# Optimization experiments

Hardware: AMD Instinct MI355X
Metric: run time of the kernel (lower is better)

## Reference

```python
import jax, jax.numpy as jnp
import numpy as np

N = 50000      # num atoms
E = 800000     # num edges
F = 64         # atom_fea_len
NBR = 64       # nbr_fea_len
NCONV = 3
T = 4096       # pooled target atoms
STATE = 2
VOCAB = 100
EPS = 1e-5


def setup_inputs() -> dict:
    key = jax.random.key(0)
    ks = jax.random.split(key, 20)
    Z = 2 * F + NBR  # concat message width
    inp = {
        "x_types": jax.random.randint(ks[0], (N,), 0, VOCAB),
        "edge_index": jax.random.randint(ks[1], (2, E), 0, N),
        "edge_attr": jax.random.normal(ks[2], (E, NBR), dtype=jnp.float32),
        "target": jax.random.randint(ks[3], (T,), 0, N),
        "emb": jax.random.normal(ks[4], (VOCAB, F), dtype=jnp.float32),
        "Wc": jax.random.normal(ks[5], (NCONV, F, Z), dtype=jnp.float32) * 0.05,
        "bc": jnp.zeros((NCONV, F), jnp.float32),
        "Wf": jax.random.normal(ks[6], (NCONV, 1, Z), dtype=jnp.float32) * 0.05,
        "bf": jnp.zeros((NCONV, 1), jnp.float32),
        "g1": jnp.ones((NCONV, F), jnp.float32),
        "b1": jnp.zeros((NCONV, F), jnp.float32),
        "g2": jnp.ones((NCONV, F), jnp.float32),
        "b2": jnp.zeros((NCONV, F), jnp.float32),
        "Wfc": jax.random.normal(ks[7], (F, F), dtype=jnp.float32) * 0.05,
        "bfc": jnp.zeros((F,), jnp.float32),
        "Ws": jax.random.normal(ks[8], (STATE, F), dtype=jnp.float32) * 0.05,
        "bs": jnp.zeros((STATE,), jnp.float32),
    }
    return inp


def _segment_softmax(logits, idx, n):
    # per-target-node softmax over variable-size edge neighborhoods
    m = jax.ops.segment_max(logits, idx, num_segments=n)
    m = jnp.where(jnp.isfinite(m), m, 0.0)
    e = jnp.exp(logits - m[idx])
    s = jax.ops.segment_sum(e, idx, num_segments=n)
    return e / (s[idx] + 1e-16)


def _batchnorm(x, gamma, beta):
    # training-mode BatchNorm1d: biased batch stats over dim 0
    mu = x.mean(0)
    var = x.var(0)
    return (x - mu) * jax.lax.rsqrt(var + EPS) * gamma + beta


def reference(x_types, edge_index, edge_attr, target, emb, Wc, bc, Wf, bf,
              g1, b1, g2, b2, Wfc, bfc, Ws, bs):
    x = emb[x_types]                      # [N, F]
    # flow='target_to_source': i = edge_index[0] (aggregate here), j = edge_index[1]
    idx_i = edge_index[0]
    idx_j = edge_index[1]
    ones = jnp.ones((edge_index.shape[1],), x.dtype)
    cnt = jax.ops.segment_sum(ones, idx_i, num_segments=x.shape[0])
    denom = jnp.maximum(cnt, 1.0)[:, None]
    for l in range(NCONV):
        z = jnp.concatenate([x[idx_i], x[idx_j], edge_attr], axis=1)  # [E, 2F+NBR]
        core = jax.nn.relu(_batchnorm(z @ Wc[l].T + bc[l], g1[l], b1[l]))  # [E, F]
        filt = (z @ Wf[l].T + bf[l])[:, 0]                                  # [E]
        alpha = _segment_softmax(filt, idx_i, x.shape[0])[:, None]          # [E, 1]
        agg = jax.ops.segment_sum(alpha * core, idx_i, num_segments=x.shape[0]) / denom
        x = jax.nn.relu(_batchnorm(agg, g2[l], b2[l]) + x)
    h = jax.nn.relu(x[target])            # [T, F]
    h = jax.nn.relu(h @ Wfc.T + bfc)
    logits = h @ Ws.T + bs                # [T, STATE]
    return jax.nn.softmax(logits, axis=-1)
```

## Files before the change

kernel.cpp:

```cpp
#include <hip/hip_runtime.h>
#include <math.h>

#define N_ATOMS 50000
#define N_EDGES 800000
#define F 64
#define Z 192
#define NCONV 3
#define T_TGT 4096
#define EPS 1e-5f
#define SLOTS 64
#define NB_SCAN 196
#define TILE_E 128
#define TPB_TILES 5
#define NBLK_MM 1250

typedef __attribute__((ext_vector_type(4))) float f32x4;
typedef __attribute__((ext_vector_type(8))) short s16x8;
typedef __attribute__((ext_vector_type(8))) __bf16 bf16x8;

static_assert(NBLK_MM * TPB_TILES * TILE_E == N_EDGES, "tiling exact");

static __device__ __forceinline__ float bf2f(unsigned short u) {
    return __uint_as_float(((unsigned int)u) << 16);
}
static __device__ __forceinline__ unsigned short f2bf(float f) {
    unsigned int u = __float_as_uint(f);
    unsigned int r = u + 0x7FFFu + ((u >> 16) & 1u);
    return (unsigned short)(r >> 16);
}
static __device__ __forceinline__ bf16x8 pack8(float4 a, float4 b) {
    s16x8 r;
    r[0] = (short)f2bf(a.x); r[1] = (short)f2bf(a.y);
    r[2] = (short)f2bf(a.z); r[3] = (short)f2bf(a.w);
    r[4] = (short)f2bf(b.x); r[5] = (short)f2bf(b.y);
    r[6] = (short)f2bf(b.z); r[7] = (short)f2bf(b.w);
    return __builtin_bit_cast(bf16x8, r);
}


__global__ void k_embed(const int* __restrict__ types, const float* __restrict__ emb,
                        float* __restrict__ x, unsigned short* __restrict__ xb) {
    int idx = blockIdx.x * 256 + threadIdx.x;
    if (idx < N_ATOMS * F) {
        int n = idx >> 6, f = idx & 63;
        float v = emb[types[n] * F + f];
        x[idx] = v;
        xb[idx] = f2bf(v);
    }
}

__global__ void k_degree(const int* __restrict__ idx_i, int* __restrict__ cnt) {
    int e = blockIdx.x * 256 + threadIdx.x;
    if (e < N_EDGES) atomicAdd(&cnt[idx_i[e]], 1);
}

__global__ void k_scanA(const int* __restrict__ cnt, int* __restrict__ bsum) {
    __shared__ int s[256];
    int base = blockIdx.x * 256, t = threadIdx.x;
    s[t] = (base + t < N_ATOMS) ? cnt[base + t] : 0;
    __syncthreads();
    for (int o = 128; o > 0; o >>= 1) {
        if (t < o) s[t] += s[t + o];
        __syncthreads();
    }
    if (t == 0) bsum[blockIdx.x] = s[0];
}

__global__ void k_scanB(int* __restrict__ bsum, int* __restrict__ rowptr) {
    __shared__ int s[256];
    int t = threadIdx.x;
    int v = (t < NB_SCAN) ? bsum[t] : 0;
    s[t] = v;
    __syncthreads();
    for (int o = 1; o < 256; o <<= 1) {
        int add = (t >= o) ? s[t - o] : 0;
        __syncthreads();
        s[t] += add;
        __syncthreads();
    }
    if (t < NB_SCAN) bsum[t] = s[t] - v;
    if (t == 0) rowptr[N_ATOMS] = N_EDGES;
}

__global__ void k_scanC(const int* __restrict__ cnt, const int* __restrict__ bsum,
                        int* __restrict__ rowptr) {
    __shared__ int s[256];
    int base = blockIdx.x * 256, t = threadIdx.x;
    int v = (base + t < N_ATOMS) ? cnt[base + t] : 0;
    s[t] = v;
    __syncthreads();
    for (int o = 1; o < 256; o <<= 1) {
        int add = (t >= o) ? s[t - o] : 0;
        __syncthreads();
        s[t] += add;
        __syncthreads();
    }
    if (base + t < N_ATOMS) rowptr[base + t] = bsum[blockIdx.x] + s[t] - v;
}

__global__ void k_scatter(const int* __restrict__ idx_i, const int* __restrict__ idx_j,
                          const int* __restrict__ rowptr, int* __restrict__ wofs,
                          int* __restrict__ i_s, int* __restrict__ j_s,
                          int* __restrict__ eperm) {
    int e = blockIdx.x * 256 + threadIdx.x;
    if (e < N_EDGES) {
        int i = idx_i[e];
        int pos = rowptr[i] + atomicAdd(&wofs[i], 1);
        i_s[pos] = i;
        j_s[pos] = idx_j[e];
        eperm[pos] = e;
    }
}

__global__ void k_ea_cvt(const float* __restrict__ ea, const int* __restrict__ eperm,
                         unsigned short* __restrict__ eab) {
    int idx = blockIdx.x * 256 + threadIdx.x;
    int row = idx >> 3;
    int seg = (idx & 7) * 8;
    if (row < N_EDGES) {
        const float* src = ea + (size_t)eperm[row] * F + seg;
        float4 a = *(const float4*)src;
        float4 b = *(const float4*)(src + 4);
        bf16x8 r = pack8(a, b);
        *(bf16x8*)(eab + (size_t)row * F + seg) = r;
    }
}

__global__ __launch_bounds__(256, 2) void k_edge_mfma(
    const unsigned short* __restrict__ xb, const unsigned short* __restrict__ eab,
    const int* __restrict__ i_s, const int* __restrict__ j_s,
    const float* __restrict__ Wc, const float* __restrict__ Wf,
    unsigned short* __restrict__ y, float* __restrict__ filt,
    float* __restrict__ stats)
{
    int t = threadIdx.x;
    int lane = t & 63, w = t >> 6;
    int c = lane & 15, g = lane >> 4;
    int goff = g * 8;

    bf16x8 Bf[6][5];
    #pragma unroll
    for (int nt = 0; nt < 4; ++nt) {
        const float* wrow = Wc + (size_t)(nt * 16 + c) * Z;
        #pragma unroll
        for (int kt = 0; kt < 6; ++kt) {
            const float* wp = wrow + kt * 32 + goff;
            float4 w0 = *(const float4*)wp;
            float4 w1 = *(const float4*)(wp + 4);
            Bf[kt][nt] = pack8(w0, w1);
        }
    }
    #pragma unroll
    for (int kt = 0; kt < 6; ++kt) {
        s16x8 zz = {0, 0, 0, 0, 0, 0, 0, 0};
        bf16x8 r = __builtin_bit_cast(bf16x8, zz);
        if (c == 0) {
            const float* wp = Wf + kt * 32 + goff;
            float4 w0 = *(const float4*)wp;
            float4 w1 = *(const float4*)(wp + 4);
            r = pack8(w0, w1);
        }
        Bf[kt][4] = r;
    }

    int tile = blockIdx.x * TPB_TILES;

    bf16x8 Af[2][6];
    #pragma unroll
    for (int m = 0; m < 2; ++m) {
        int e = tile * TILE_E + (w * 2 + m) * 16 + c;
        const unsigned short* bi = xb + (size_t)i_s[e] * F + goff;
        const unsigned short* bj = xb + (size_t)j_s[e] * F + goff;
        const unsigned short* be = eab + (size_t)e * F + goff;
        Af[m][0] = *(const bf16x8*)(bi);
        Af[m][1] = *(const bf16x8*)(bi + 32);
        Af[m][2] = *(const bf16x8*)(bj);
        Af[m][3] = *(const bf16x8*)(bj + 32);
        Af[m][4] = *(const bf16x8*)(be);
        Af[m][5] = *(const bf16x8*)(be + 32);
    }

    float ssum[4] = {0.f, 0.f, 0.f, 0.f};
    float ssq[4]  = {0.f, 0.f, 0.f, 0.f};

    for (int it = 0; it < TPB_TILES; ++it) {
        int cur = tile + it;
        int nxt = (it + 1 < TPB_TILES) ? cur + 1 : cur;
        const unsigned short *bi2[2], *bj2[2], *be2[2];
        #pragma unroll
        for (int m = 0; m < 2; ++m) {
            int e = nxt * TILE_E + (w * 2 + m) * 16 + c;
            bi2[m] = xb + (size_t)i_s[e] * F + goff;
            bj2[m] = xb + (size_t)j_s[e] * F + goff;
            be2[m] = eab + (size_t)e * F + goff;
        }

        f32x4 acc[2][5];
        #pragma unroll
        for (int m = 0; m < 2; ++m)
            #pragma unroll
            for (int nt = 0; nt < 5; ++nt)
                acc[m][nt] = (f32x4){0.f, 0.f, 0.f, 0.f};

        #pragma unroll
        for (int kt = 0; kt < 6; ++kt) {
            #pragma unroll
            for (int m = 0; m < 2; ++m) {
                #pragma unroll
                for (int nt = 0; nt < 5; ++nt)
                    acc[m][nt] = __builtin_amdgcn_mfma_f32_16x16x32_bf16(
                        Af[m][kt], Bf[kt][nt], acc[m][nt], 0, 0, 0);
            }
            #pragma unroll
            for (int m = 0; m < 2; ++m) {
                const unsigned short* p = (kt < 2) ? bi2[m] : (kt < 4) ? bj2[m] : be2[m];
                Af[m][kt] = *(const bf16x8*)(p + (kt & 1) * 32);
            }
        }

        #pragma unroll
        for (int m = 0; m < 2; ++m) {
            int ebase = cur * TILE_E + (w * 2 + m) * 16 + g * 4;
            #pragma unroll
            for (int nt = 0; nt < 4; ++nt) {
                #pragma unroll
                for (int q = 0; q < 4; ++q) {
                    float v = acc[m][nt][q];
                    y[(size_t)(ebase + q) * F + nt * 16 + c] = f2bf(v);
                    ssum[nt] += v;
                    ssq[nt] += v * v;
                }
            }
            if (c == 0) {
                #pragma unroll
                for (int q = 0; q < 4; ++q) filt[ebase + q] = acc[m][4][q];
            }
        }
    }

    int slot = (blockIdx.x & (SLOTS - 1)) * 128;
    #pragma unroll
    for (int nt = 0; nt < 4; ++nt) {
        float S = ssum[nt], Q = ssq[nt];
        S += __shfl_xor(S, 16, 64); S += __shfl_xor(S, 32, 64);
        Q += __shfl_xor(Q, 16, 64); Q += __shfl_xor(Q, 32, 64);
        if (g == 0) {
            atomicAdd(&stats[slot + nt * 16 + c], S);
            atomicAdd(&stats[slot + 64 + nt * 16 + c], Q);
        }
    }
}


__global__ void k_finbn(const float* __restrict__ stats, float* __restrict__ bnp, float count) {
    int f = threadIdx.x;
    float S = 0.f, Q = 0.f;
    for (int s = 0; s < SLOTS; ++s) {
        S += stats[s * 128 + f];
        Q += stats[s * 128 + 64 + f];
    }
    float mu = S / count;
    float var = Q / count - mu * mu;
    var = fmaxf(var, 0.f);
    bnp[f] = mu;
    bnp[64 + f] = 1.f / sqrtf(var + EPS);
}

__global__ __launch_bounds__(256) void k_node_agg(
    const unsigned short* __restrict__ y, const float* __restrict__ filt,
    const int* __restrict__ rowptr, const int* __restrict__ cnt,
    const float* __restrict__ bnp, const float* __restrict__ g1, const float* __restrict__ b1,
    float* __restrict__ agg)
{
    int t = threadIdx.x;
    int lane = t & 63;
    int node = blockIdx.x * 4 + (t >> 6);
    if (node >= N_ATOMS) return;
    int beg = rowptr[node], end = rowptr[node + 1];
    float mu = bnp[lane], rstd = bnp[64 + lane];
    float ga = g1[lane], be = b1[lane];
    float fm = -INFINITY;
    for (int i = beg + lane; i < end; i += 64) fm = fmaxf(fm, filt[i]);
    #pragma unroll
    for (int o = 32; o > 0; o >>= 1) fm = fmaxf(fm, __shfl_xor(fm, o, 64));
    float acc = 0.f, ssum = 0.f;
    for (int e = beg; e < end; ++e) {
        float wgt = expf(filt[e] - fm);
        float yv = bf2f(y[(size_t)e * F + lane]);
        float core = fmaxf((yv - mu) * rstd * ga + be, 0.f);
        acc += wgt * core;
        ssum += wgt;
    }
    float dn = fmaxf((float)cnt[node], 1.f);
    agg[(size_t)node * F + lane] = acc / (ssum + 1e-16f) / dn;
}

__global__ void k_colstats(const float* __restrict__ agg, float* __restrict__ stats) {
    __shared__ float buf[4][64];
    int t = threadIdx.x;
    int f = t & 63, g = t >> 6;
    float S = 0.f, Q = 0.f;
    for (int n = blockIdx.x * 4 + g; n < N_ATOMS; n += gridDim.x * 4) {
        float v = agg[(size_t)n * F + f];
        S += v; Q += v * v;
    }
    buf[g][f] = S;
    __syncthreads();
    if (t < 64) {
        float s2 = buf[0][t] + buf[1][t] + buf[2][t] + buf[3][t];
        atomicAdd(&stats[(blockIdx.x & 63) * 128 + t], s2);
    }
    __syncthreads();
    buf[g][f] = Q;
    __syncthreads();
    if (t < 64) {
        float q2 = buf[0][t] + buf[1][t] + buf[2][t] + buf[3][t];
        atomicAdd(&stats[(blockIdx.x & 63) * 128 + 64 + t], q2);
    }
}

__global__ void k_node_upd(const float* __restrict__ agg, const float* __restrict__ bnp,
                           const float* __restrict__ g2, const float* __restrict__ b2,
                           const float* __restrict__ xin, float* __restrict__ xout,
                           unsigned short* __restrict__ xbout) {
    int idx = blockIdx.x * 256 + threadIdx.x;
    if (idx < N_ATOMS * F) {
        int f = idx & 63;
        float v = (agg[idx] - bnp[f]) * bnp[64 + f] * g2[f] + b2[f] + xin[idx];
        v = fmaxf(v, 0.f);
        xout[idx] = v;
        xbout[idx] = f2bf(v);
    }
}


__global__ __launch_bounds__(256) void k_head(
    const float* __restrict__ x, const int* __restrict__ target,
    const float* __restrict__ Wfc, const float* __restrict__ bfc,
    const float* __restrict__ Ws, const float* __restrict__ bs,
    float* __restrict__ out)
{
    __shared__ float hbuf[4][64];
    int t = threadIdx.x;
    int lane = t & 63, w = t >> 6;
    int tt = blockIdx.x * 4 + w;
    int a = target[min(tt, T_TGT - 1)];
    float h = fmaxf(x[(size_t)a * F + lane], 0.f);
    hbuf[w][lane] = h;
    __syncthreads();
    float acc = bfc[lane];
    #pragma unroll 8
    for (int k = 0; k < F; ++k) acc += hbuf[w][k] * Wfc[lane * F + k];
    float h2 = fmaxf(acc, 0.f);
    float p0 = h2 * Ws[lane];
    float p1 = h2 * Ws[F + lane];
    #pragma unroll
    for (int o = 32; o > 0; o >>= 1) {
        p0 += __shfl_xor(p0, o, 64);
        p1 += __shfl_xor(p1, o, 64);
    }
    if (lane == 0 && tt < T_TGT) {
        float l0 = p0 + bs[0], l1 = p1 + bs[1];
        float mx = fmaxf(l0, l1);
        float e0v = expf(l0 - mx), e1v = expf(l1 - mx);
        float inv = 1.f / (e0v + e1v);
        out[tt * 2 + 0] = e0v * inv;
        out[tt * 2 + 1] = e1v * inv;
    }
}


extern "C" void kernel_launch(void* const* d_in, const int* in_sizes, int n_in,
                              void* d_out, int out_size, void* d_ws, size_t ws_size,
                              hipStream_t stream)
{
    const int*   x_types = (const int*)d_in[0];
    const int*   eidx    = (const int*)d_in[1];
    const float* ea      = (const float*)d_in[2];
    const int*   target  = (const int*)d_in[3];
    const float* emb     = (const float*)d_in[4];
    const float* Wc      = (const float*)d_in[5];
    const float* Wf      = (const float*)d_in[7];
    const float* g1      = (const float*)d_in[9];
    const float* b1      = (const float*)d_in[10];
    const float* g2      = (const float*)d_in[11];
    const float* b2      = (const float*)d_in[12];
    const float* Wfc     = (const float*)d_in[13];
    const float* bfc     = (const float*)d_in[14];
    const float* Ws      = (const float*)d_in[15];
    const float* bs      = (const float*)d_in[16];
    float* out = (float*)d_out;
    const int* idx_i = eidx;
    const int* idx_j = eidx + N_EDGES;

    char* p = (char*)d_ws;
    auto alloc = [&](size_t bytes) {
        char* r = p;
        p += (bytes + 255) & ~(size_t)255;
        return r;
    };
    float* xa            = (float*)alloc((size_t)N_ATOMS * F * 4);
    float* xb_f          = (float*)alloc((size_t)N_ATOMS * F * 4);
    unsigned short* x16a = (unsigned short*)alloc((size_t)N_ATOMS * F * 2);
    unsigned short* x16b = (unsigned short*)alloc((size_t)N_ATOMS * F * 2);
    unsigned short* eab  = (unsigned short*)alloc((size_t)N_EDGES * F * 2);
    unsigned short* ybuf = (unsigned short*)alloc((size_t)N_EDGES * F * 2);
    float* filt          = (float*)alloc((size_t)N_EDGES * 4);
    float* agg           = (float*)alloc((size_t)N_ATOMS * F * 4);
    int* cnt             = (int*)alloc((size_t)N_ATOMS * 4);
    int* rowptr          = (int*)alloc((size_t)(N_ATOMS + 1) * 4);
    int* wofs            = (int*)alloc((size_t)N_ATOMS * 4);
    int* i_s             = (int*)alloc((size_t)N_EDGES * 4);
    int* j_s             = (int*)alloc((size_t)N_EDGES * 4);
    int* eperm           = (int*)alloc((size_t)N_EDGES * 4);
    int* bsum            = (int*)alloc(256 * 4);
    float* stats         = (float*)alloc(SLOTS * 128 * 4);
    float* bnp1          = (float*)alloc(128 * 4);
    float* bnp2          = (float*)alloc(128 * 4);
    (void)ws_size; (void)in_sizes; (void)n_in; (void)out_size;

    hipMemsetAsync(cnt, 0, (size_t)N_ATOMS * 4, stream);
    hipMemsetAsync(wofs, 0, (size_t)N_ATOMS * 4, stream);
    k_embed<<<(N_ATOMS * F + 255) / 256, 256, 0, stream>>>(x_types, emb, xa, x16a);
    k_degree<<<(N_EDGES + 255) / 256, 256, 0, stream>>>(idx_i, cnt);
    k_scanA<<<NB_SCAN, 256, 0, stream>>>(cnt, bsum);
    k_scanB<<<1, 256, 0, stream>>>(bsum, rowptr);
    k_scanC<<<NB_SCAN, 256, 0, stream>>>(cnt, bsum, rowptr);
    k_scatter<<<(N_EDGES + 255) / 256, 256, 0, stream>>>(idx_i, idx_j, rowptr, wofs,
                                                         i_s, j_s, eperm);
    k_ea_cvt<<<(N_EDGES * 8 + 255) / 256, 256, 0, stream>>>(ea, eperm, eab);

    float* xcur = xa;
    float* xnxt = xb_f;
    unsigned short* x16cur = x16a;
    unsigned short* x16nxt = x16b;
    for (int l = 0; l < NCONV; ++l) {
        hipMemsetAsync(stats, 0, SLOTS * 128 * 4, stream);
        k_edge_mfma<<<NBLK_MM, 256, 0, stream>>>(
            x16cur, eab, i_s, j_s,
            Wc + (size_t)l * F * Z, Wf + (size_t)l * Z,
            ybuf, filt, stats);
        k_finbn<<<1, 64, 0, stream>>>(stats, bnp1, (float)N_EDGES);
        k_node_agg<<<N_ATOMS / 4, 256, 0, stream>>>(ybuf, filt, rowptr, cnt, bnp1,
                                                    g1 + (size_t)l * F, b1 + (size_t)l * F, agg);
        hipMemsetAsync(stats, 0, SLOTS * 128 * 4, stream);
        k_colstats<<<256, 256, 0, stream>>>(agg, stats);
        k_finbn<<<1, 64, 0, stream>>>(stats, bnp2, (float)N_ATOMS);
        k_node_upd<<<(N_ATOMS * F + 255) / 256, 256, 0, stream>>>(
            agg, bnp2, g2 + (size_t)l * F, b2 + (size_t)l * F, xcur, xnxt, x16nxt);
        float* tf = xcur; xcur = xnxt; xnxt = tf;
        unsigned short* ts = x16cur; x16cur = x16nxt; x16nxt = ts;
    }
    k_head<<<T_TGT / 4, 256, 0, stream>>>(xcur, target, Wfc, bfc, Ws, bs, out);
}
```

Measured before the change: 858.9 us.

## Decompose filter logit per node/edge, stage weights in LDS, coalesce y stores

The filter logit is split into per-node terms (pi, pj) and a per-edge term (pe). The per-edge term is computed once for all layers in a fused prep kernel, which removes the fifth MFMA column tile. Wc B-fragments now sit in LDS instead of registers, and launch bounds rise to 3 blocks per SM. y stores go through a swizzled LDS transpose so they leave as coalesced 16-byte rows, and node_agg processes 4 edges per wavefront with vectorized loads. The filter now comes from fp32 dot products rather than bf16 MFMA, and the extra LDS reads and small kernels add their own cost.

```diff
diff --git a/kernel.cpp b/kernel.cpp
--- a/kernel.cpp
+++ b/kernel.cpp
@@ -112,72 +112,99 @@
     }
 }
 
-__global__ void k_ea_cvt(const float* __restrict__ ea, const int* __restrict__ eperm,
-                         unsigned short* __restrict__ eab) {
-    int idx = blockIdx.x * 256 + threadIdx.x;
-    int row = idx >> 3;
-    int seg = (idx & 7) * 8;
-    if (row < N_EDGES) {
-        const float* src = ea + (size_t)eperm[row] * F + seg;
-        float4 a = *(const float4*)src;
-        float4 b = *(const float4*)(src + 4);
-        bf16x8 r = pack8(a, b);
-        *(bf16x8*)(eab + (size_t)row * F + seg) = r;
-    }
-}
-
-__global__ __launch_bounds__(256, 2) void k_edge_mfma(
+__global__ void k_prep(const float* __restrict__ ea, const int* __restrict__ eperm,
+                       const float* __restrict__ Wf,
+                       unsigned short* __restrict__ eab, float* __restrict__ pe) {
+    int row = blockIdx.x * 256 + threadIdx.x;
+    if (row >= N_EDGES) return;
+    const float* src = ea + (size_t)eperm[row] * F;
+    float d0 = 0.f, d1 = 0.f, d2 = 0.f;
+    #pragma unroll
+    for (int ch = 0; ch < 8; ++ch) {
+        float4 a = *(const float4*)(src + ch * 8);
+        float4 b = *(const float4*)(src + ch * 8 + 4);
+        float vv[8] = {a.x, a.y, a.z, a.w, b.x, b.y, b.z, b.w};
+        #pragma unroll
+        for (int j = 0; j < 8; ++j) {
+            int k = 128 + ch * 8 + j;
+            d0 += vv[j] * Wf[k];
+            d1 += vv[j] * Wf[Z + k];
+            d2 += vv[j] * Wf[2 * Z + k];
+        }
+        *(bf16x8*)(eab + (size_t)row * F + ch * 8) = pack8(a, b);
+    }
+    pe[row] = d0;
+    pe[N_EDGES + row] = d1;
+    pe[2 * N_EDGES + row] = d2;
+}
+
+__global__ void k_pij(const float* __restrict__ x, const float* __restrict__ Wf,
+                      float* __restrict__ pi, float* __restrict__ pj) {
+    int n = blockIdx.x * 256 + threadIdx.x;
+    if (n >= N_ATOMS) return;
+    const float* xr = x + (size_t)n * F;
+    float di = 0.f, dj = 0.f;
+    #pragma unroll
+    for (int ch = 0; ch < 16; ++ch) {
+        float4 a = *(const float4*)(xr + ch * 4);
+        di += a.x * Wf[ch * 4] + a.y * Wf[ch * 4 + 1] + a.z * Wf[ch * 4 + 2] + a.w * Wf[ch * 4 + 3];
+        dj += a.x * Wf[64 + ch * 4] + a.y * Wf[64 + ch * 4 + 1] + a.z * Wf[64 + ch * 4 + 2] + a.w * Wf[64 + ch * 4 + 3];
+    }
+    pi[n] = di;
+    pj[n] = dj;
+}
+
+__global__ __launch_bounds__(256, 3) void k_edge_mfma(
     const unsigned short* __restrict__ xb, const unsigned short* __restrict__ eab,
     const int* __restrict__ i_s, const int* __restrict__ j_s,
-    const float* __restrict__ Wc, const float* __restrict__ Wf,
+    const float* __restrict__ Wc,
+    const float* __restrict__ pi, const float* __restrict__ pj, const float* __restrict__ pe,
     unsigned short* __restrict__ y, float* __restrict__ filt,
     float* __restrict__ stats)
 {
+    __shared__ unsigned short BfL[24 * 64 * 8];
+    __shared__ unsigned short TW[4][16 * 64];
+
     int t = threadIdx.x;
     int lane = t & 63, w = t >> 6;
     int c = lane & 15, g = lane >> 4;
     int goff = g * 8;
 
-    bf16x8 Bf[6][5];
-    #pragma unroll
-    for (int nt = 0; nt < 4; ++nt) {
-        const float* wrow = Wc + (size_t)(nt * 16 + c) * Z;
-        #pragma unroll
-        for (int kt = 0; kt < 6; ++kt) {
-            const float* wp = wrow + kt * 32 + goff;
-            float4 w0 = *(const float4*)wp;
-            float4 w1 = *(const float4*)(wp + 4);
-            Bf[kt][nt] = pack8(w0, w1);
-        }
-    }
-    #pragma unroll
-    for (int kt = 0; kt < 6; ++kt) {
-        s16x8 zz = {0, 0, 0, 0, 0, 0, 0, 0};
-        bf16x8 r = __builtin_bit_cast(bf16x8, zz);
-        if (c == 0) {
-            const float* wp = Wf + kt * 32 + goff;
-            float4 w0 = *(const float4*)wp;
-            float4 w1 = *(const float4*)(wp + 4);
-            r = pack8(w0, w1);
-        }
-        Bf[kt][4] = r;
-    }
+    #pragma unroll
+    for (int rep = 0; rep < 6; ++rep) {
+        int idx = rep * 256 + t;
+        int fr = idx >> 6, ln = idx & 63;
+        int kt = fr >> 2, nt = fr & 3;
+        int cc = ln & 15, gg = ln >> 4;
+        int kb = kt * 32 + gg * 8;
+        int okb = (kb < 64) ? (kb + 128) : (kb - 64);
+        const float* wp = Wc + (size_t)(nt * 16 + cc) * Z + okb;
+        float4 w0 = *(const float4*)wp;
+        float4 w1 = *(const float4*)(wp + 4);
+        *(bf16x8*)(BfL + (size_t)idx * 8) = pack8(w0, w1);
+    }
+    __syncthreads();
 
     int tile = blockIdx.x * TPB_TILES;
-
     bf16x8 Af[2][6];
+    int iN[2], jN[2];
+
     #pragma unroll
     for (int m = 0; m < 2; ++m) {
         int e = tile * TILE_E + (w * 2 + m) * 16 + c;
-        const unsigned short* bi = xb + (size_t)i_s[e] * F + goff;
-        const unsigned short* bj = xb + (size_t)j_s[e] * F + goff;
+        int ic = i_s[e], jc = j_s[e];
         const unsigned short* be = eab + (size_t)e * F + goff;
-        Af[m][0] = *(const bf16x8*)(bi);
-        Af[m][1] = *(const bf16x8*)(bi + 32);
-        Af[m][2] = *(const bf16x8*)(bj);
-        Af[m][3] = *(const bf16x8*)(bj + 32);
-        Af[m][4] = *(const bf16x8*)(be);
-        Af[m][5] = *(const bf16x8*)(be + 32);
+        const unsigned short* bi = xb + (size_t)ic * F + goff;
+        const unsigned short* bj = xb + (size_t)jc * F + goff;
+        Af[m][0] = *(const bf16x8*)(be);
+        Af[m][1] = *(const bf16x8*)(be + 32);
+        Af[m][2] = *(const bf16x8*)(bi);
+        Af[m][3] = *(const bf16x8*)(bi + 32);
+        Af[m][4] = *(const bf16x8*)(bj);
+        Af[m][5] = *(const bf16x8*)(bj + 32);
+        int e1 = min((tile + 1) * TILE_E + (w * 2 + m) * 16 + c, N_EDGES - 1);
+        iN[m] = i_s[e1];
+        jN[m] = j_s[e1];
     }
 
     float ssum[4] = {0.f, 0.f, 0.f, 0.f};
@@ -185,57 +212,81 @@
 
     for (int it = 0; it < TPB_TILES; ++it) {
         int cur = tile + it;
-        int nxt = (it + 1 < TPB_TILES) ? cur + 1 : cur;
-        const unsigned short *bi2[2], *bj2[2], *be2[2];
+        int eN[2], iF[2], jF[2];
         #pragma unroll
         for (int m = 0; m < 2; ++m) {
-            int e = nxt * TILE_E + (w * 2 + m) * 16 + c;
-            bi2[m] = xb + (size_t)i_s[e] * F + goff;
-            bj2[m] = xb + (size_t)j_s[e] * F + goff;
-            be2[m] = eab + (size_t)e * F + goff;
+            eN[m] = min((cur + 1) * TILE_E + (w * 2 + m) * 16 + c, N_EDGES - 1);
+            int e2 = min((cur + 2) * TILE_E + (w * 2 + m) * 16 + c, N_EDGES - 1);
+            iF[m] = i_s[e2];
+            jF[m] = j_s[e2];
         }
-
-        f32x4 acc[2][5];
+        int ii = 0, jj = 0, er = 0;
+        float pv = 0.f;
+        if (lane < 32) {
+            er = cur * TILE_E + w * 32 + lane;
+            ii = i_s[er];
+            jj = j_s[er];
+            pv = pe[er];
+        }
+
+        f32x4 acc[2][4];
         #pragma unroll
         for (int m = 0; m < 2; ++m)
             #pragma unroll
-            for (int nt = 0; nt < 5; ++nt)
+            for (int nt = 0; nt < 4; ++nt)
                 acc[m][nt] = (f32x4){0.f, 0.f, 0.f, 0.f};
 
         #pragma unroll
         for (int kt = 0; kt < 6; ++kt) {
+            const unsigned short* bbase = BfL + (size_t)(kt * 4) * 512 + lane * 8;
+            bf16x8 b0 = *(const bf16x8*)(bbase);
+            bf16x8 b1 = *(const bf16x8*)(bbase + 512);
+            bf16x8 b2 = *(const bf16x8*)(bbase + 1024);
+            bf16x8 b3 = *(const bf16x8*)(bbase + 1536);
             #pragma unroll
             for (int m = 0; m < 2; ++m) {
-                #pragma unroll
-                for (int nt = 0; nt < 5; ++nt)
-                    acc[m][nt] = __builtin_amdgcn_mfma_f32_16x16x32_bf16(
-                        Af[m][kt], Bf[kt][nt], acc[m][nt], 0, 0, 0);
+                acc[m][0] = __builtin_amdgcn_mfma_f32_16x16x32_bf16(Af[m][kt], b0, acc[m][0], 0, 0, 0);
+                acc[m][1] = __builtin_amdgcn_mfma_f32_16x16x32_bf16(Af[m][kt], b1, acc[m][1], 0, 0, 0);
+                acc[m][2] = __builtin_amdgcn_mfma_f32_16x16x32_bf16(Af[m][kt], b2, acc[m][2], 0, 0, 0);
+                acc[m][3] = __builtin_amdgcn_mfma_f32_16x16x32_bf16(Af[m][kt], b3, acc[m][3], 0, 0, 0);
             }
             #pragma unroll
             for (int m = 0; m < 2; ++m) {
-                const unsigned short* p = (kt < 2) ? bi2[m] : (kt < 4) ? bj2[m] : be2[m];
-                Af[m][kt] = *(const bf16x8*)(p + (kt & 1) * 32);
+                const unsigned short* p =
+                    (kt < 2) ? (eab + (size_t)eN[m] * F)
+                  : (kt < 4) ? (xb + (size_t)iN[m] * F)
+                             : (xb + (size_t)jN[m] * F);
+                Af[m][kt] = *(const bf16x8*)(p + goff + ((kt & 1) << 5));
             }
         }
 
+        unsigned short* tw = &TW[w][0];
         #pragma unroll
         for (int m = 0; m < 2; ++m) {
-            int ebase = cur * TILE_E + (w * 2 + m) * 16 + g * 4;
             #pragma unroll
             for (int nt = 0; nt < 4; ++nt) {
+                int cl = nt * 2 + (c >> 3);
+                int u = c & 7;
                 #pragma unroll
                 for (int q = 0; q < 4; ++q) {
                     float v = acc[m][nt][q];
-                    y[(size_t)(ebase + q) * F + nt * 16 + c] = f2bf(v);
                     ssum[nt] += v;
                     ssq[nt] += v * v;
+                    int r = g * 4 + q;
+                    tw[r * 64 + ((cl ^ (r & 7)) << 3) + u] = f2bf(v);
                 }
             }
-            if (c == 0) {
-                #pragma unroll
-                for (int q = 0; q < 4; ++q) filt[ebase + q] = acc[m][4][q];
+            #pragma unroll
+            for (int ps = 0; ps < 2; ++ps) {
+                int r = ps * 8 + (lane >> 3);
+                bf16x8 v = *(const bf16x8*)(tw + r * 64 + (((lane & 7) ^ (r & 7)) << 3));
+                *(bf16x8*)(y + (size_t)(cur * TILE_E + w * 32 + m * 16 + r) * F + (lane & 7) * 8) = v;
             }
         }
+        if (lane < 32) filt[er] = pi[ii] + pj[jj] + pv;
+
+        iN[0] = iF[0]; iN[1] = iF[1];
+        jN[0] = jF[0]; jN[1] = jF[1];
     }
 
     int slot = (blockIdx.x & (SLOTS - 1)) * 128;
@@ -275,24 +326,46 @@
     int t = threadIdx.x;
     int lane = t & 63;
     int node = blockIdx.x * 4 + (t >> 6);
-    if (node >= N_ATOMS) return;
     int beg = rowptr[node], end = rowptr[node + 1];
-    float mu = bnp[lane], rstd = bnp[64 + lane];
-    float ga = g1[lane], be = b1[lane];
+    int es = lane >> 4, fq = lane & 15;
+    float4 mu4 = *(const float4*)(bnp + fq * 4);
+    float4 rs4 = *(const float4*)(bnp + 64 + fq * 4);
+    float4 ga4 = *(const float4*)(g1 + fq * 4);
+    float4 be4 = *(const float4*)(b1 + fq * 4);
+
     float fm = -INFINITY;
     for (int i = beg + lane; i < end; i += 64) fm = fmaxf(fm, filt[i]);
     #pragma unroll
     for (int o = 32; o > 0; o >>= 1) fm = fmaxf(fm, __shfl_xor(fm, o, 64));
-    float acc = 0.f, ssum = 0.f;
-    for (int e = beg; e < end; ++e) {
-        float wgt = expf(filt[e] - fm);
-        float yv = bf2f(y[(size_t)e * F + lane]);
-        float core = fmaxf((yv - mu) * rstd * ga + be, 0.f);
-        acc += wgt * core;
-        ssum += wgt;
-    }
-    float dn = fmaxf((float)cnt[node], 1.f);
-    agg[(size_t)node * F + lane] = acc / (ssum + 1e-16f) / dn;
+
+    float a0 = 0.f, a1 = 0.f, a2 = 0.f, a3 = 0.f, ss = 0.f;
+    for (int base = beg; base < end; base += 4) {
+        int ee = base + es;
+        int eec = min(ee, end - 1);
+        float wgt = (ee < end) ? expf(filt[eec] - fm) : 0.f;
+        ushort4 yv = *(const ushort4*)(y + (size_t)eec * F + fq * 4);
+        float c0 = fmaxf((bf2f(yv.x) - mu4.x) * rs4.x * ga4.x + be4.x, 0.f);
+        float c1 = fmaxf((bf2f(yv.y) - mu4.y) * rs4.y * ga4.y + be4.y, 0.f);
+        float c2 = fmaxf((bf2f(yv.z) - mu4.z) * rs4.z * ga4.z + be4.z, 0.f);
+        float c3 = fmaxf((bf2f(yv.w) - mu4.w) * rs4.w * ga4.w + be4.w, 0.f);
+        a0 += wgt * c0; a1 += wgt * c1; a2 += wgt * c2; a3 += wgt * c3;
+        ss += wgt;
+    }
+    #pragma unroll
+    for (int o = 16; o <= 32; o <<= 1) {
+        a0 += __shfl_xor(a0, o, 64);
+        a1 += __shfl_xor(a1, o, 64);
+        a2 += __shfl_xor(a2, o, 64);
+        a3 += __shfl_xor(a3, o, 64);
+        ss += __shfl_xor(ss, o, 64);
+    }
+    if (lane < 16) {
+        float dn = fmaxf((float)cnt[node], 1.f);
+        float inv = 1.f / ((ss + 1e-16f) * dn);
+        float4 o4;
+        o4.x = a0 * inv; o4.y = a1 * inv; o4.z = a2 * inv; o4.w = a3 * inv;
+        *(float4*)(agg + (size_t)node * F + fq * 4) = o4;
+    }
 }
 
 __global__ void k_colstats(const float* __restrict__ agg, float* __restrict__ stats) {
@@ -406,6 +479,9 @@
     unsigned short* eab  = (unsigned short*)alloc((size_t)N_EDGES * F * 2);
     unsigned short* ybuf = (unsigned short*)alloc((size_t)N_EDGES * F * 2);
     float* filt          = (float*)alloc((size_t)N_EDGES * 4);
+    float* pe            = (float*)alloc((size_t)NCONV * N_EDGES * 4);
+    float* pi            = (float*)alloc((size_t)N_ATOMS * 4);
+    float* pj            = (float*)alloc((size_t)N_ATOMS * 4);
     float* agg           = (float*)alloc((size_t)N_ATOMS * F * 4);
     int* cnt             = (int*)alloc((size_t)N_ATOMS * 4);
     int* rowptr          = (int*)alloc((size_t)(N_ATOMS + 1) * 4);
@@ -428,17 +504,19 @@
     k_scanC<<<NB_SCAN, 256, 0, stream>>>(cnt, bsum, rowptr);
     k_scatter<<<(N_EDGES + 255) / 256, 256, 0, stream>>>(idx_i, idx_j, rowptr, wofs,
                                                          i_s, j_s, eperm);
-    k_ea_cvt<<<(N_EDGES * 8 + 255) / 256, 256, 0, stream>>>(ea, eperm, eab);
+    k_prep<<<N_EDGES / 256, 256, 0, stream>>>(ea, eperm, Wf, eab, pe);
 
     float* xcur = xa;
     float* xnxt = xb_f;
     unsigned short* x16cur = x16a;
     unsigned short* x16nxt = x16b;
     for (int l = 0; l < NCONV; ++l) {
+        k_pij<<<(N_ATOMS + 255) / 256, 256, 0, stream>>>(xcur, Wf + (size_t)l * Z, pi, pj);
         hipMemsetAsync(stats, 0, SLOTS * 128 * 4, stream);
         k_edge_mfma<<<NBLK_MM, 256, 0, stream>>>(
             x16cur, eab, i_s, j_s,
-            Wc + (size_t)l * F * Z, Wf + (size_t)l * Z,
+            Wc + (size_t)l * F * Z,
+            pi, pj, pe + (size_t)l * N_EDGES,
             ybuf, filt, stats);
         k_finbn<<<1, 64, 0, stream>>>(stats, bnp1, (float)N_EDGES);
         k_node_agg<<<N_ATOMS / 4, 256, 0, stream>>>(ybuf, filt, rowptr, cnt, bnp1,
```

After: 996.0 us. 16.0% more time.
